# Kernel tuning notes

Hardware: AMD Instinct MI355X
Metric: run time of the kernel (lower is better)

The kernel has to match this reference:

```python
import jax, jax.numpy as jnp
import numpy as np

B, C, H, W = 512, 3, 64, 32
K = 2                      # fractional pool kernel size
HOUT, WOUT = 38, 16        # floor(64*0.6), floor(32*0.5)
HID = 128                  # RNN hidden size
D = C * HOUT               # RNN input size = 114


def _frac_starts(in_size, out_size, k, u=0.5):
    # PyTorch fractional-max-pool interval formula with deterministic sample u
    alpha = (in_size - k) / (out_size - 1)
    i = np.arange(out_size - 1)
    starts = np.floor((i + u) * alpha) - np.floor(u * alpha)
    return np.concatenate([starts, [in_size - k]]).astype(np.int32)

ROW = _frac_starts(H, HOUT, K)   # (HOUT,) window start rows
COL = _frac_starts(W, WOUT, K)   # (WOUT,) window start cols


def setup_inputs() -> dict:
    key = jax.random.key(0)
    ks = jax.random.split(key, 5)
    s = 1.0 / np.sqrt(HID)  # torch RNNCell init scale
    return {
        "x": jax.random.normal(ks[0], (B, C, H, W), jnp.float32),
        "W_ih": jax.random.uniform(ks[1], (HID, D), jnp.float32, -s, s),
        "W_hh": jax.random.uniform(ks[2], (HID, HID), jnp.float32, -s, s),
        "b_ih": jax.random.uniform(ks[3], (HID,), jnp.float32, -s, s),
        "b_hh": jax.random.uniform(ks[4], (HID,), jnp.float32, -s, s),
    }


def reference(x, W_ih, W_hh, b_ih, b_hh):
    # 1) fractional max pool, kernel 2: pairwise max over gathered window starts
    xr = jnp.maximum(x[:, :, ROW, :], x[:, :, ROW + 1, :])          # (B,C,HOUT,W)
    pooled = jnp.maximum(xr[:, :, :, COL], xr[:, :, :, COL + 1])    # (B,C,HOUT,WOUT)
    # 2) exact (erf-based) GELU, matching torch nn.GELU default
    act = jax.nn.gelu(pooled, approximate=False)
    # 3) sequence over width: (WOUT, B, C*HOUT), C-major flatten matches torch view
    seq = act.transpose(3, 0, 1, 2).reshape(WOUT, B, D)
    # 4) vanilla RNNCell across time via scan
    def step(h, xt):
        h = jnp.tanh(xt @ W_ih.T + b_ih + h @ W_hh.T + b_hh)
        return h, h
    _, outs = jax.lax.scan(step, jnp.zeros((B, HID), x.dtype), seq)  # (WOUT,B,HID)
    # 5) temporal mean + tanh
    t_mean = jnp.tanh(outs.mean(axis=0))                             # (B,HID)
    # 6) modulate by global spatial mean of pooled; torch broadcasting of
    #    (B,HID) * (B,1,1,1) yields (B,1,B,HID) — replicated faithfully
    s_mean = pooled.mean(axis=(1, 2, 3), keepdims=True)              # (B,1,1,1)
    return t_mean * s_mean                                           # (B,1,B,HID)
```

## Files before the change

kernel.cpp:

```cpp
#include <hip/hip_runtime.h>
#include <math.h>

#define BB   512
#define CC   3
#define HH   64
#define WW   32
#define HOUT 38
#define WOUT 16
#define HID  128
#define DD   114
#define SEQP 120
#define WIHP 120
#define WHHP 132
#define NPOOL (CC*HOUT*WOUT)

typedef float f32x4 __attribute__((ext_vector_type(4)));

__device__ __forceinline__ float fast_tanh(float u) {
    return 1.f - 2.f / (__expf(2.f * u) + 1.f);
}

#define WS_SMEAN 0
#define WS_TMEAN 512

__global__ __launch_bounds__(256, 2)
void k1_fused(const float* __restrict__ x,
              const float* __restrict__ Wih,
              const float* __restrict__ Whh,
              const float* __restrict__ bih,
              const float* __restrict__ bhh,
              float* __restrict__ s_mean,
              float* __restrict__ t_mean)
{
    __shared__ __align__(16) float wst[HID * WHHP];
    __shared__ __align__(16) float seq[WOUT][SEQP];
    __shared__ __align__(16) float hbuf[2][HID];
    __shared__ float red[4];
    __shared__ int   rowl[HOUT];

    const int tid  = threadIdx.x;
    const int wid  = tid >> 6;
    const int lane = tid & 63;
    const int kl   = (wid << 5) | (lane & 31);
    const int kc   = lane >> 5;
    const int b    = blockIdx.x;

    f32x4 xpf[6];
    {
        const f32x4* xg = (const f32x4*)(x + (size_t)b * (CC*HH*WW));
        #pragma unroll
        for (int i = 0; i < 6; ++i) xpf[i] = xg[tid + 256*i];
    }
    f32x4 wihpf[14], wihtail;
    {
        const f32x4* wg = (const f32x4*)Wih;
        #pragma unroll
        for (int i = 0; i < 14; ++i) wihpf[i] = wg[tid + 256*i];
        if (tid < 64) wihtail = wg[3584 + tid];
    }

    if (tid < HOUT) {
        double alpha = (double)(HH - 2) / (double)(HOUT - 1);
        rowl[tid] = (tid < HOUT - 1)
            ? (int)(floor((tid + 0.5) * alpha) - floor(0.5 * alpha))
            : (HH - 2);
    }
    if (tid < HID) hbuf[0][tid] = 0.f;
    if (tid < 96)  seq[tid / 6][DD + tid % 6] = 0.f;

    {
        f32x4* xd = (f32x4*)wst;
        #pragma unroll
        for (int i = 0; i < 6; ++i) xd[tid + 256*i] = xpf[i];
    }
    __syncthreads();

    float ps = 0.f;
    #pragma unroll
    for (int it = 0; it < 8; ++it) {
        int idx = tid + it*256;
        if (idx < NPOOL) {
            int c  = idx / (HOUT*WOUT);
            int r  = idx % (HOUT*WOUT);
            int ho = r / WOUT;
            int wo = r % WOUT;
            const float* p0 = &wst[c*(HH*WW) + rowl[ho]*WW + 2*wo];
            float m = fmaxf(fmaxf(p0[0], p0[1]), fmaxf(p0[WW], p0[WW+1]));
            ps += m;
            seq[wo][c*HOUT + ho] =
                0.5f * m * (1.f + erff(m * 0.70710678118654752440f));
        }
    }
    #pragma unroll
    for (int off = 32; off > 0; off >>= 1) ps += __shfl_down(ps, off);
    if (lane == 0) red[wid] = ps;
    __syncthreads();
    if (tid == 0)
        s_mean[b] = (red[0] + red[1] + red[2] + red[3]) * (1.f / (float)NPOOL);

    #pragma unroll
    for (int i = 0; i < 14; ++i) {
        int j = 4*(tid + 256*i);
        #pragma unroll
        for (int e = 0; e < 4; ++e) {
            int r  = (j + e) / DD;
            int cc = (j + e) - r*DD;
            wst[r*WIHP + cc] = wihpf[i][e];
        }
    }
    if (tid < 64) {
        int j = 4*(3584 + tid);
        #pragma unroll
        for (int e = 0; e < 4; ++e) {
            int r  = (j + e) / DD;
            int cc = (j + e) - r*DD;
            wst[r*WIHP + cc] = wihtail[e];
        }
    }
    for (int j = tid; j < HID*6; j += 256)
        wst[(j/6)*WIHP + DD + (j % 6)] = 0.f;
    __syncthreads();

    f32x4 wih[15];
    {
        const f32x4* wr = (const f32x4*)&wst[kl*WIHP + kc*60];
        #pragma unroll
        for (int dd = 0; dd < 15; ++dd) wih[dd] = wr[dd];
    }

    f32x4 whhpf[16];
    {
        const f32x4* hg = (const f32x4*)Whh;
        #pragma unroll
        for (int i = 0; i < 16; ++i) whhpf[i] = hg[tid + 256*i];
    }

    float zreg[WOUT];
    #pragma unroll
    for (int t = 0; t < WOUT; ++t) {
        const f32x4* a4 = (const f32x4*)&seq[t][kc*60];
        float s0 = 0.f, s1 = 0.f, s2 = 0.f, s3 = 0.f;
        #pragma unroll
        for (int dd = 0; dd < 15; ++dd) {
            f32x4 a = a4[dd];
            s0 = fmaf(wih[dd].x, a.x, s0);
            s1 = fmaf(wih[dd].y, a.y, s1);
            s2 = fmaf(wih[dd].z, a.z, s2);
            s3 = fmaf(wih[dd].w, a.w, s3);
        }
        float p = (s0 + s1) + (s2 + s3);
        zreg[t] = p + __shfl_xor(p, 32);
    }
    {
        const float bias = bih[kl] + bhh[kl];
        #pragma unroll
        for (int t = 0; t < WOUT; ++t) zreg[t] += bias;
    }
    __syncthreads();

    #pragma unroll
    for (int i = 0; i < 16; ++i) {
        int j4 = tid + 256*i;
        *(f32x4*)&wst[(j4 >> 5)*WHHP + ((j4 & 31) << 2)] = whhpf[i];
    }
    __syncthreads();
    f32x4 whh[16];
    {
        const f32x4* wr = (const f32x4*)&wst[kl*WHHP + (kc << 6)];
        #pragma unroll
        for (int dd = 0; dd < 16; ++dd) whh[dd] = wr[dd];
    }

    float hsum = 0.f;
    #pragma unroll
    for (int t = 0; t < WOUT; ++t) {
        const int cur = t & 1, nxt = cur ^ 1;
        const f32x4* h4 = (const f32x4*)&hbuf[cur][kc << 6];
        float s0 = 0.f, s1 = 0.f, s2 = 0.f, s3 = 0.f;
        #pragma unroll
        for (int dd = 0; dd < 16; ++dd) {
            f32x4 hv = h4[dd];
            s0 = fmaf(whh[dd].x, hv.x, s0);
            s1 = fmaf(whh[dd].y, hv.y, s1);
            s2 = fmaf(whh[dd].z, hv.z, s2);
            s3 = fmaf(whh[dd].w, hv.w, s3);
        }
        float p  = (s0 + s1) + (s2 + s3);
        float u  = zreg[t] + p + __shfl_xor(p, 32);
        float hn = fast_tanh(u);
        hsum += hn;
        if (kc == 0) hbuf[nxt][kl] = hn;
        __syncthreads();
    }
    if (kc == 0) t_mean[b*HID + kl] = fast_tanh(hsum * (1.f / 16.f));
}

__global__ __launch_bounds__(256)
void k2_out(const float* __restrict__ s_mean,
            const float* __restrict__ t_mean,
            f32x4* __restrict__ out)
{
    const int i   = blockIdx.x >> 3;
    const int sub = blockIdx.x & 7;
    const float s = s_mean[i];
    const f32x4* t4 = (const f32x4*)t_mean + sub*2048;
    f32x4*       o  = out + (size_t)i*16384 + sub*2048;
    const int tid = threadIdx.x;
    #pragma unroll
    for (int j = 0; j < 8; ++j) {
        int idx = tid + j*256;
        o[idx] = s * t4[idx];
    }
}

extern "C" void kernel_launch(void* const* d_in, const int* in_sizes, int n_in,
                              void* d_out, int out_size, void* d_ws, size_t ws_size,
                              hipStream_t stream)
{
    const float* x   = (const float*)d_in[0];
    const float* Wih = (const float*)d_in[1];
    const float* Whh = (const float*)d_in[2];
    const float* bih = (const float*)d_in[3];
    const float* bhh = (const float*)d_in[4];

    float* ws     = (float*)d_ws;
    float* s_mean = ws + WS_SMEAN;
    float* t_mean = ws + WS_TMEAN;

    k1_fused<<<dim3(BB), dim3(256), 0, stream>>>(x, Wih, Whh, bih, bhh, s_mean, t_mean);
    k2_out  <<<dim3(4096), dim3(256), 0, stream>>>(s_mean, t_mean, (f32x4*)d_out);
}
```

Baseline: 48.46 us.

## Process two batch elements per block to amortize weight staging

Each block of the fused pool+GELU+RNN kernel now handles two batch samples instead of one, halving the grid to 256 blocks. The Wih/Whh weight loads, the shared-memory transposes and the per-step barriers are shared across both samples, and the two independent recurrences interleave to hide FMA and LDS latency. The cost is more registers (launch bounds drop to one block per SM) and fewer blocks than CUs on a 256-CU device, so occupancy and parallelism shrink.

```diff
diff --git a/kernel.cpp b/kernel.cpp
--- a/kernel.cpp
+++ b/kernel.cpp
@@ -13,6 +13,7 @@
 #define WIHP 120
 #define WHHP 132
 #define NPOOL (CC*HOUT*WOUT)
+#define XPAIR (2*CC*HH*WW)
 
 typedef float f32x4 __attribute__((ext_vector_type(4)));
 
@@ -23,7 +24,7 @@
 #define WS_SMEAN 0
 #define WS_TMEAN 512
 
-__global__ __launch_bounds__(256, 2)
+__global__ __launch_bounds__(256, 1)
 void k1_fused(const float* __restrict__ x,
               const float* __restrict__ Wih,
               const float* __restrict__ Whh,
@@ -33,9 +34,11 @@
               float* __restrict__ t_mean)
 {
     __shared__ __align__(16) float wst[HID * WHHP];
-    __shared__ __align__(16) float seq[WOUT][SEQP];
-    __shared__ __align__(16) float hbuf[2][HID];
-    __shared__ float red[4];
+    __shared__ __align__(16) float seq0[WOUT][SEQP];
+    __shared__ __align__(16) float seq1[WOUT][SEQP];
+    __shared__ __align__(16) float hb0[2][HID];
+    __shared__ __align__(16) float hb1[2][HID];
+    __shared__ float red[2][4];
     __shared__ int   rowl[HOUT];
 
     const int tid  = threadIdx.x;
@@ -43,13 +46,13 @@
     const int lane = tid & 63;
     const int kl   = (wid << 5) | (lane & 31);
     const int kc   = lane >> 5;
-    const int b    = blockIdx.x;
-
-    f32x4 xpf[6];
-    {
-        const f32x4* xg = (const f32x4*)(x + (size_t)b * (CC*HH*WW));
-        #pragma unroll
-        for (int i = 0; i < 6; ++i) xpf[i] = xg[tid + 256*i];
+    const int b0   = 2 * blockIdx.x;
+
+    f32x4 xpf[12];
+    {
+        const f32x4* xg = (const f32x4*)(x + (size_t)b0 * (CC*HH*WW));
+        #pragma unroll
+        for (int i = 0; i < 12; ++i) xpf[i] = xg[tid + 256*i];
     }
     f32x4 wihpf[14], wihtail;
     {
@@ -65,38 +68,47 @@
             ? (int)(floor((tid + 0.5) * alpha) - floor(0.5 * alpha))
             : (HH - 2);
     }
-    if (tid < HID) hbuf[0][tid] = 0.f;
-    if (tid < 96)  seq[tid / 6][DD + tid % 6] = 0.f;
+    if (tid < HID) { hb0[0][tid] = 0.f; hb1[0][tid] = 0.f; }
+    if (tid < 96) {
+        seq0[tid / 6][DD + tid % 6] = 0.f;
+        seq1[tid / 6][DD + tid % 6] = 0.f;
+    }
 
     {
         f32x4* xd = (f32x4*)wst;
         #pragma unroll
-        for (int i = 0; i < 6; ++i) xd[tid + 256*i] = xpf[i];
-    }
-    __syncthreads();
-
-    float ps = 0.f;
-    #pragma unroll
-    for (int it = 0; it < 8; ++it) {
+        for (int i = 0; i < 12; ++i) xd[tid + 256*i] = xpf[i];
+    }
+    __syncthreads();
+
+    float ps0 = 0.f, ps1 = 0.f;
+    #pragma unroll
+    for (int it = 0; it < 15; ++it) {
         int idx = tid + it*256;
-        if (idx < NPOOL) {
-            int c  = idx / (HOUT*WOUT);
-            int r  = idx % (HOUT*WOUT);
+        if (idx < 2*NPOOL) {
+            int bsel = (idx >= NPOOL);
+            int r0   = idx - bsel*NPOOL;
+            int c  = r0 / (HOUT*WOUT);
+            int r  = r0 % (HOUT*WOUT);
             int ho = r / WOUT;
             int wo = r % WOUT;
-            const float* p0 = &wst[c*(HH*WW) + rowl[ho]*WW + 2*wo];
+            const float* p0 = &wst[bsel*(CC*HH*WW) + c*(HH*WW) + rowl[ho]*WW + 2*wo];
             float m = fmaxf(fmaxf(p0[0], p0[1]), fmaxf(p0[WW], p0[WW+1]));
-            ps += m;
-            seq[wo][c*HOUT + ho] =
-                0.5f * m * (1.f + erff(m * 0.70710678118654752440f));
-        }
-    }
-    #pragma unroll
-    for (int off = 32; off > 0; off >>= 1) ps += __shfl_down(ps, off);
-    if (lane == 0) red[wid] = ps;
-    __syncthreads();
-    if (tid == 0)
-        s_mean[b] = (red[0] + red[1] + red[2] + red[3]) * (1.f / (float)NPOOL);
+            float a = 0.5f * m * (1.f + erff(m * 0.70710678118654752440f));
+            if (bsel) { ps1 += m; seq1[wo][c*HOUT + ho] = a; }
+            else      { ps0 += m; seq0[wo][c*HOUT + ho] = a; }
+        }
+    }
+    #pragma unroll
+    for (int off = 32; off > 0; off >>= 1) {
+        ps0 += __shfl_down(ps0, off);
+        ps1 += __shfl_down(ps1, off);
+    }
+    if (lane == 0) { red[0][wid] = ps0; red[1][wid] = ps1; }
+    __syncthreads();
+    if (tid < 2)
+        s_mean[b0 + tid] = (red[tid][0] + red[tid][1] + red[tid][2] + red[tid][3])
+                           * (1.f / (float)NPOOL);
 
     #pragma unroll
     for (int i = 0; i < 14; ++i) {
@@ -135,26 +147,30 @@
         for (int i = 0; i < 16; ++i) whhpf[i] = hg[tid + 256*i];
     }
 
-    float zreg[WOUT];
+    float zr0[WOUT], zr1[WOUT];
     #pragma unroll
     for (int t = 0; t < WOUT; ++t) {
-        const f32x4* a4 = (const f32x4*)&seq[t][kc*60];
+        const f32x4* a4 = (const f32x4*)&seq0[t][kc*60];
+        const f32x4* c4 = (const f32x4*)&seq1[t][kc*60];
         float s0 = 0.f, s1 = 0.f, s2 = 0.f, s3 = 0.f;
+        float u0 = 0.f, u1 = 0.f, u2 = 0.f, u3 = 0.f;
         #pragma unroll
         for (int dd = 0; dd < 15; ++dd) {
-            f32x4 a = a4[dd];
-            s0 = fmaf(wih[dd].x, a.x, s0);
-            s1 = fmaf(wih[dd].y, a.y, s1);
-            s2 = fmaf(wih[dd].z, a.z, s2);
-            s3 = fmaf(wih[dd].w, a.w, s3);
+            f32x4 a = a4[dd], c = c4[dd], w = wih[dd];
+            s0 = fmaf(w.x, a.x, s0); u0 = fmaf(w.x, c.x, u0);
+            s1 = fmaf(w.y, a.y, s1); u1 = fmaf(w.y, c.y, u1);
+            s2 = fmaf(w.z, a.z, s2); u2 = fmaf(w.z, c.z, u2);
+            s3 = fmaf(w.w, a.w, s3); u3 = fmaf(w.w, c.w, u3);
         }
         float p = (s0 + s1) + (s2 + s3);
-        zreg[t] = p + __shfl_xor(p, 32);
+        float q = (u0 + u1) + (u2 + u3);
+        zr0[t] = p + __shfl_xor(p, 32);
+        zr1[t] = q + __shfl_xor(q, 32);
     }
     {
         const float bias = bih[kl] + bhh[kl];
         #pragma unroll
-        for (int t = 0; t < WOUT; ++t) zreg[t] += bias;
+        for (int t = 0; t < WOUT; ++t) { zr0[t] += bias; zr1[t] += bias; }
     }
     __syncthreads();
 
@@ -171,28 +187,36 @@
         for (int dd = 0; dd < 16; ++dd) whh[dd] = wr[dd];
     }
 
-    float hsum = 0.f;
+    float hsum0 = 0.f, hsum1 = 0.f;
     #pragma unroll
     for (int t = 0; t < WOUT; ++t) {
         const int cur = t & 1, nxt = cur ^ 1;
-        const f32x4* h4 = (const f32x4*)&hbuf[cur][kc << 6];
+        const f32x4* h40 = (const f32x4*)&hb0[cur][kc << 6];
+        const f32x4* h41 = (const f32x4*)&hb1[cur][kc << 6];
         float s0 = 0.f, s1 = 0.f, s2 = 0.f, s3 = 0.f;
+        float u0 = 0.f, u1 = 0.f, u2 = 0.f, u3 = 0.f;
         #pragma unroll
         for (int dd = 0; dd < 16; ++dd) {
-            f32x4 hv = h4[dd];
-            s0 = fmaf(whh[dd].x, hv.x, s0);
-            s1 = fmaf(whh[dd].y, hv.y, s1);
-            s2 = fmaf(whh[dd].z, hv.z, s2);
-            s3 = fmaf(whh[dd].w, hv.w, s3);
+            f32x4 hv = h40[dd], gv = h41[dd], w = whh[dd];
+            s0 = fmaf(w.x, hv.x, s0); u0 = fmaf(w.x, gv.x, u0);
+            s1 = fmaf(w.y, hv.y, s1); u1 = fmaf(w.y, gv.y, u1);
+            s2 = fmaf(w.z, hv.z, s2); u2 = fmaf(w.z, gv.z, u2);
+            s3 = fmaf(w.w, hv.w, s3); u3 = fmaf(w.w, gv.w, u3);
         }
         float p  = (s0 + s1) + (s2 + s3);
-        float u  = zreg[t] + p + __shfl_xor(p, 32);
-        float hn = fast_tanh(u);
-        hsum += hn;
-        if (kc == 0) hbuf[nxt][kl] = hn;
+        float q  = (u0 + u1) + (u2 + u3);
+        float v0 = zr0[t] + p + __shfl_xor(p, 32);
+        float v1 = zr1[t] + q + __shfl_xor(q, 32);
+        float hn0 = fast_tanh(v0);
+        float hn1 = fast_tanh(v1);
+        hsum0 += hn0; hsum1 += hn1;
+        if (kc == 0) { hb0[nxt][kl] = hn0; hb1[nxt][kl] = hn1; }
         __syncthreads();
     }
-    if (kc == 0) t_mean[b*HID + kl] = fast_tanh(hsum * (1.f / 16.f));
+    if (kc == 0) {
+        t_mean[(b0    )*HID + kl] = fast_tanh(hsum0 * (1.f / 16.f));
+        t_mean[(b0 + 1)*HID + kl] = fast_tanh(hsum1 * (1.f / 16.f));
+    }
 }
 
 __global__ __launch_bounds__(256)
@@ -227,6 +251,6 @@
     float* s_mean = ws + WS_SMEAN;
     float* t_mean = ws + WS_TMEAN;
 
-    k1_fused<<<dim3(BB), dim3(256), 0, stream>>>(x, Wih, Whh, bih, bhh, s_mean, t_mean);
+    k1_fused<<<dim3(BB/2), dim3(256), 0, stream>>>(x, Wih, Whh, bih, bhh, s_mean, t_mean);
     k2_out  <<<dim3(4096), dim3(256), 0, stream>>>(s_mean, t_mean, (f32x4*)d_out);
 }
```

Result: slower. 55.10 us (+13.7%).

## Double RNN block to 512 threads with 4-way split dot products

Applied to the files above, without the earlier changes.

Moves the fused pool+RNN kernel from 256 to 512 threads per batch row. Each hidden unit's input and recurrent dot products are now split across four 32-wide chunks instead of two 64-wide ones, reduced with two cross-lane shuffles. The seq and hidden buffers are padded to a 36-float stride per 32-element chunk to spread LDS banks. The aim is to shorten the serial per-step recurrence and cut per-thread register weight storage, at the cost of one more shuffle per step and more threads waiting at each barrier.

```diff
diff --git a/kernel.cpp b/kernel.cpp
--- a/kernel.cpp
+++ b/kernel.cpp
@@ -9,8 +9,9 @@
 #define WOUT 16
 #define HID  128
 #define DD   114
-#define SEQP 120
-#define WIHP 120
+#define SEQQ 36
+#define SEQP 144
+#define WIHP 132
 #define WHHP 132
 #define NPOOL (CC*HOUT*WOUT)
 
@@ -23,7 +24,7 @@
 #define WS_SMEAN 0
 #define WS_TMEAN 512
 
-__global__ __launch_bounds__(256, 2)
+__global__ __launch_bounds__(512, 4)
 void k1_fused(const float* __restrict__ x,
               const float* __restrict__ Wih,
               const float* __restrict__ Whh,
@@ -34,28 +35,28 @@
 {
     __shared__ __align__(16) float wst[HID * WHHP];
     __shared__ __align__(16) float seq[WOUT][SEQP];
-    __shared__ __align__(16) float hbuf[2][HID];
-    __shared__ float red[4];
+    __shared__ __align__(16) float hbuf[2][SEQP];
+    __shared__ float red[8];
     __shared__ int   rowl[HOUT];
 
     const int tid  = threadIdx.x;
     const int wid  = tid >> 6;
     const int lane = tid & 63;
-    const int kl   = (wid << 5) | (lane & 31);
-    const int kc   = lane >> 5;
+    const int kl   = (wid << 4) | (lane & 15);
+    const int kc   = lane >> 4;
     const int b    = blockIdx.x;
 
-    f32x4 xpf[6];
+    f32x4 xpf[3];
     {
         const f32x4* xg = (const f32x4*)(x + (size_t)b * (CC*HH*WW));
         #pragma unroll
-        for (int i = 0; i < 6; ++i) xpf[i] = xg[tid + 256*i];
-    }
-    f32x4 wihpf[14], wihtail;
+        for (int i = 0; i < 3; ++i) xpf[i] = xg[tid + 512*i];
+    }
+    f32x4 wihpf[7], wihtail;
     {
         const f32x4* wg = (const f32x4*)Wih;
         #pragma unroll
-        for (int i = 0; i < 14; ++i) wihpf[i] = wg[tid + 256*i];
+        for (int i = 0; i < 7; ++i) wihpf[i] = wg[tid + 512*i];
         if (tid < 64) wihtail = wg[3584 + tid];
     }
 
@@ -65,20 +66,23 @@
             ? (int)(floor((tid + 0.5) * alpha) - floor(0.5 * alpha))
             : (HH - 2);
     }
-    if (tid < HID) hbuf[0][tid] = 0.f;
-    if (tid < 96)  seq[tid / 6][DD + tid % 6] = 0.f;
+    if (tid < HID) hbuf[0][SEQQ*(tid >> 5) + (tid & 31)] = 0.f;
+    if (tid < 224) {
+        int t = tid / 14, o = 18 + tid % 14;
+        seq[t][3*SEQQ + o] = 0.f;
+    }
 
     {
         f32x4* xd = (f32x4*)wst;
         #pragma unroll
-        for (int i = 0; i < 6; ++i) xd[tid + 256*i] = xpf[i];
+        for (int i = 0; i < 3; ++i) xd[tid + 512*i] = xpf[i];
     }
     __syncthreads();
 
     float ps = 0.f;
     #pragma unroll
-    for (int it = 0; it < 8; ++it) {
-        int idx = tid + it*256;
+    for (int it = 0; it < 4; ++it) {
+        int idx = tid + it*512;
         if (idx < NPOOL) {
             int c  = idx / (HOUT*WOUT);
             int r  = idx % (HOUT*WOUT);
@@ -87,7 +91,8 @@
             const float* p0 = &wst[c*(HH*WW) + rowl[ho]*WW + 2*wo];
             float m = fmaxf(fmaxf(p0[0], p0[1]), fmaxf(p0[WW], p0[WW+1]));
             ps += m;
-            seq[wo][c*HOUT + ho] =
+            int d = c*HOUT + ho;
+            seq[wo][SEQQ*(d >> 5) + (d & 31)] =
                 0.5f * m * (1.f + erff(m * 0.70710678118654752440f));
         }
     }
@@ -95,12 +100,16 @@
     for (int off = 32; off > 0; off >>= 1) ps += __shfl_down(ps, off);
     if (lane == 0) red[wid] = ps;
     __syncthreads();
-    if (tid == 0)
-        s_mean[b] = (red[0] + red[1] + red[2] + red[3]) * (1.f / (float)NPOOL);
-
-    #pragma unroll
-    for (int i = 0; i < 14; ++i) {
-        int j = 4*(tid + 256*i);
+    if (tid == 0) {
+        float r = 0.f;
+        #pragma unroll
+        for (int i = 0; i < 8; ++i) r += red[i];
+        s_mean[b] = r * (1.f / (float)NPOOL);
+    }
+
+    #pragma unroll
+    for (int i = 0; i < 7; ++i) {
+        int j = 4*(tid + 512*i);
         #pragma unroll
         for (int e = 0; e < 4; ++e) {
             int r  = (j + e) / DD;
@@ -117,38 +126,39 @@
             wst[r*WIHP + cc] = wihtail[e];
         }
     }
-    for (int j = tid; j < HID*6; j += 256)
-        wst[(j/6)*WIHP + DD + (j % 6)] = 0.f;
-    __syncthreads();
-
-    f32x4 wih[15];
-    {
-        const f32x4* wr = (const f32x4*)&wst[kl*WIHP + kc*60];
-        #pragma unroll
-        for (int dd = 0; dd < 15; ++dd) wih[dd] = wr[dd];
-    }
-
-    f32x4 whhpf[16];
+    for (int j = tid; j < HID*14; j += 512)
+        wst[(j/14)*WIHP + DD + (j % 14)] = 0.f;
+    __syncthreads();
+
+    f32x4 wih[8];
+    {
+        const f32x4* wr = (const f32x4*)&wst[kl*WIHP + (kc << 5)];
+        #pragma unroll
+        for (int dd = 0; dd < 8; ++dd) wih[dd] = wr[dd];
+    }
+
+    f32x4 whhpf[8];
     {
         const f32x4* hg = (const f32x4*)Whh;
         #pragma unroll
-        for (int i = 0; i < 16; ++i) whhpf[i] = hg[tid + 256*i];
+        for (int i = 0; i < 8; ++i) whhpf[i] = hg[tid + 512*i];
     }
 
     float zreg[WOUT];
     #pragma unroll
     for (int t = 0; t < WOUT; ++t) {
-        const f32x4* a4 = (const f32x4*)&seq[t][kc*60];
+        const f32x4* a4 = (const f32x4*)&seq[t][kc*SEQQ];
         float s0 = 0.f, s1 = 0.f, s2 = 0.f, s3 = 0.f;
         #pragma unroll
-        for (int dd = 0; dd < 15; ++dd) {
-            f32x4 a = a4[dd];
-            s0 = fmaf(wih[dd].x, a.x, s0);
-            s1 = fmaf(wih[dd].y, a.y, s1);
-            s2 = fmaf(wih[dd].z, a.z, s2);
-            s3 = fmaf(wih[dd].w, a.w, s3);
+        for (int dd = 0; dd < 8; ++dd) {
+            f32x4 a = a4[dd], w = wih[dd];
+            s0 = fmaf(w.x, a.x, s0);
+            s1 = fmaf(w.y, a.y, s1);
+            s2 = fmaf(w.z, a.z, s2);
+            s3 = fmaf(w.w, a.w, s3);
         }
         float p = (s0 + s1) + (s2 + s3);
+        p += __shfl_xor(p, 16);
         zreg[t] = p + __shfl_xor(p, 32);
     }
     {
@@ -159,37 +169,38 @@
     __syncthreads();
 
     #pragma unroll
-    for (int i = 0; i < 16; ++i) {
-        int j4 = tid + 256*i;
+    for (int i = 0; i < 8; ++i) {
+        int j4 = tid + 512*i;
         *(f32x4*)&wst[(j4 >> 5)*WHHP + ((j4 & 31) << 2)] = whhpf[i];
     }
     __syncthreads();
-    f32x4 whh[16];
-    {
-        const f32x4* wr = (const f32x4*)&wst[kl*WHHP + (kc << 6)];
-        #pragma unroll
-        for (int dd = 0; dd < 16; ++dd) whh[dd] = wr[dd];
+    f32x4 whh[8];
+    {
+        const f32x4* wr = (const f32x4*)&wst[kl*WHHP + (kc << 5)];
+        #pragma unroll
+        for (int dd = 0; dd < 8; ++dd) whh[dd] = wr[dd];
     }
 
     float hsum = 0.f;
     #pragma unroll
     for (int t = 0; t < WOUT; ++t) {
         const int cur = t & 1, nxt = cur ^ 1;
-        const f32x4* h4 = (const f32x4*)&hbuf[cur][kc << 6];
+        const f32x4* h4 = (const f32x4*)&hbuf[cur][kc*SEQQ];
         float s0 = 0.f, s1 = 0.f, s2 = 0.f, s3 = 0.f;
         #pragma unroll
-        for (int dd = 0; dd < 16; ++dd) {
-            f32x4 hv = h4[dd];
-            s0 = fmaf(whh[dd].x, hv.x, s0);
-            s1 = fmaf(whh[dd].y, hv.y, s1);
-            s2 = fmaf(whh[dd].z, hv.z, s2);
-            s3 = fmaf(whh[dd].w, hv.w, s3);
-        }
-        float p  = (s0 + s1) + (s2 + s3);
+        for (int dd = 0; dd < 8; ++dd) {
+            f32x4 hv = h4[dd], w = whh[dd];
+            s0 = fmaf(w.x, hv.x, s0);
+            s1 = fmaf(w.y, hv.y, s1);
+            s2 = fmaf(w.z, hv.z, s2);
+            s3 = fmaf(w.w, hv.w, s3);
+        }
+        float p = (s0 + s1) + (s2 + s3);
+        p += __shfl_xor(p, 16);
         float u  = zreg[t] + p + __shfl_xor(p, 32);
         float hn = fast_tanh(u);
         hsum += hn;
-        if (kc == 0) hbuf[nxt][kl] = hn;
+        if (kc == 0) hbuf[nxt][SEQQ*(kl >> 5) + (kl & 31)] = hn;
         __syncthreads();
     }
     if (kc == 0) t_mean[b*HID + kl] = fast_tanh(hsum * (1.f / 16.f));
@@ -227,6 +238,6 @@
     float* s_mean = ws + WS_SMEAN;
     float* t_mean = ws + WS_TMEAN;
 
-    k1_fused<<<dim3(BB), dim3(256), 0, stream>>>(x, Wih, Whh, bih, bhh, s_mean, t_mean);
+    k1_fused<<<dim3(BB), dim3(512), 0, stream>>>(x, Wih, Whh, bih, bhh, s_mean, t_mean);
     k2_out  <<<dim3(4096), dim3(256), 0, stream>>>(s_mean, t_mean, (f32x4*)d_out);
 }
```

Measured after the change: 48.48 us. About the same (+0.0%).
